# Kernel optimization log

Measured on AMD Instinct MI355X. Metric: run time of the kernel, lower is better.

Reference implementation:

```python
import jax, jax.numpy as jnp
import numpy as np

NEG_INF = -1e9  # masked_fill value from the torch module


def setup_inputs() -> dict:
    key = jax.random.key(0)
    ks = jax.random.split(key, 6)
    n_edges, hidden = 100000, 256
    n_paths, max_len = 20000, 16
    edge_emb = jax.random.normal(ks[0], (n_edges, hidden), dtype=jnp.float32)
    paths = jax.random.randint(ks[1], (n_paths, max_len), 0, n_edges)
    path_lens = jax.random.randint(ks[2], (n_paths,), 0, max_len)  # +1 in reference -> 1..max_len
    path_mask = jax.random.randint(ks[3], (n_paths,), 0, 2)
    # nn.Linear(hidden, 1) parameters
    W = jax.random.normal(ks[4], (1, hidden), dtype=jnp.float32) / np.sqrt(hidden)
    b = jax.random.normal(ks[5], (1,), dtype=jnp.float32) * 0.01
    return {"edge_emb": edge_emb, "paths": paths, "path_lens": path_lens,
            "path_mask": path_mask, "W": W, "b": b, "deterministic": 1}


def reference(edge_emb, paths, path_lens, path_mask, W, b, deterministic):
    # ragged per-path mean: emulate `for p in paths: edge_emb[p].mean(0)` with padded gather
    lens = path_lens + 1                                   # [P], 1..max_len
    pos = jnp.arange(paths.shape[1])                        # [L]
    valid = pos[None, :] < lens[:, None]                    # [P, L]
    gathered = edge_emb[paths]                              # [P, L, H]
    z = jnp.sum(jnp.where(valid[..., None], gathered, 0.0), axis=1) / lens[:, None].astype(edge_emb.dtype)  # [P, H]
    logits = z @ W[0] + b[0]                                # [P]  (Linear(H,1).squeeze())
    logits = jnp.where(path_mask == 0, NEG_INF, logits)
    logp = jax.nn.log_softmax(logits)
    if deterministic:
        p = jnp.argmax(logits)
    else:
        p = jax.random.categorical(jax.random.key(42), logits)
    logprob = logp[p]
    return (p, logprob, z[p])
```

## Files before the change

### kernel.cpp

```cpp
#include <hip/hip_runtime.h>
#include <math.h>

#define NEG_INF -1e9f

__global__ __launch_bounds__(256) void k_edge_dot(
    const float* __restrict__ emb, const float* __restrict__ W,
    float* __restrict__ s, int n_edges)
{
    int wave = (blockIdx.x * (int)blockDim.x + (int)threadIdx.x) >> 6;
    int lane = threadIdx.x & 63;
    if (wave >= n_edges) return;
    const float4 e = ((const float4*)emb)[wave * 64 + lane];
    const float4 w = ((const float4*)W)[lane];
    float d = e.x * w.x + e.y * w.y + e.z * w.z + e.w * w.w;
#pragma unroll
    for (int off = 32; off; off >>= 1) d += __shfl_down(d, off, 64);
    if (lane == 0) s[wave] = d;
}

__global__ __launch_bounds__(256) void k_logits16(
    const float* __restrict__ s, const int* __restrict__ paths,
    const int* __restrict__ path_lens, const int* __restrict__ path_mask,
    const float* __restrict__ b, float* __restrict__ logits, int n_paths)
{
    int p = blockIdx.x * (int)blockDim.x + (int)threadIdx.x;
    if (p >= n_paths) return;
    if (path_mask[p] == 0) { logits[p] = NEG_INF; return; }
    int len = path_lens[p] + 1;
    const int4* pp4 = (const int4*)(paths + (size_t)p * 16);
    int4 a0 = pp4[0], a1 = pp4[1], a2 = pp4[2], a3 = pp4[3];
    int idx[16] = { a0.x, a0.y, a0.z, a0.w, a1.x, a1.y, a1.z, a1.w,
                    a2.x, a2.y, a2.z, a2.w, a3.x, a3.y, a3.z, a3.w };
    float acc = 0.f;
#pragma unroll
    for (int j = 0; j < 16; ++j) {
        float v = s[idx[j]];
        acc += (j < len) ? v : 0.f;
    }
    logits[p] = acc / (float)len + b[0];
}

__global__ __launch_bounds__(256) void k_logits_gen(
    const float* __restrict__ s, const int* __restrict__ paths,
    const int* __restrict__ path_lens, const int* __restrict__ path_mask,
    const float* __restrict__ b, float* __restrict__ logits,
    int n_paths, int max_len)
{
    int p = blockIdx.x * (int)blockDim.x + (int)threadIdx.x;
    if (p >= n_paths) return;
    if (path_mask[p] == 0) { logits[p] = NEG_INF; return; }
    int len = path_lens[p] + 1;
    const int* pp = paths + (size_t)p * max_len;
    float acc = 0.f;
    for (int j = 0; j < len; ++j) acc += s[pp[j]];
    logits[p] = acc / (float)len + b[0];
}

__global__ __launch_bounds__(1024) void k_final(
    const float* __restrict__ logits, const float* __restrict__ emb,
    const int* __restrict__ paths, const int* __restrict__ path_lens,
    float* __restrict__ out, int n_paths, int max_len)
{
    __shared__ float sv[16];
    __shared__ int   si[16];
    __shared__ float ssum[16];
    __shared__ int   s_p, s_len;
    __shared__ float s_max, s_logprob;

    int tid = threadIdx.x, lane = tid & 63, wv = tid >> 6;
    int n4 = n_paths >> 2;
    const float4* l4 = (const float4*)logits;

    float bv = -INFINITY; int bi = 0x7fffffff;
    for (int i = tid; i < n4; i += 1024) {
        float4 v = l4[i];
        int base = i << 2;
        if (v.x > bv) { bv = v.x; bi = base; }
        if (v.y > bv) { bv = v.y; bi = base + 1; }
        if (v.z > bv) { bv = v.z; bi = base + 2; }
        if (v.w > bv) { bv = v.w; bi = base + 3; }
    }
    for (int i = (n4 << 2) + tid; i < n_paths; i += 1024) {
        float v = logits[i];
        if (v > bv) { bv = v; bi = i; }
    }
#pragma unroll
    for (int off = 32; off; off >>= 1) {
        float ov = __shfl_down(bv, off, 64);
        int   oi = __shfl_down(bi, off, 64);
        if (ov > bv || (ov == bv && oi < bi)) { bv = ov; bi = oi; }
    }
    if (lane == 0) { sv[wv] = bv; si[wv] = bi; }
    __syncthreads();
    if (tid == 0) {
        float mv = sv[0]; int mi = si[0];
        for (int w = 1; w < 16; ++w)
            if (sv[w] > mv || (sv[w] == mv && si[w] < mi)) { mv = sv[w]; mi = si[w]; }
        s_max = mv; s_p = mi; s_len = path_lens[mi] + 1;
    }
    __syncthreads();
    float mx = s_max;

    float se = 0.f;
    for (int i = tid; i < n4; i += 1024) {
        float4 v = l4[i];
        se += expf(v.x - mx) + expf(v.y - mx) + expf(v.z - mx) + expf(v.w - mx);
    }
    for (int i = (n4 << 2) + tid; i < n_paths; i += 1024)
        se += expf(logits[i] - mx);
#pragma unroll
    for (int off = 32; off; off >>= 1) se += __shfl_down(se, off, 64);
    if (lane == 0) ssum[wv] = se;
    __syncthreads();
    if (tid == 0) {
        float t = 0.f;
        for (int w = 0; w < 16; ++w) t += ssum[w];
        s_logprob = -logf(t);
    }
    __syncthreads();

    int p = s_p, len = s_len;
    if (tid < 256) {
        const int* pp = paths + (size_t)p * max_len;
        float acc = 0.f;
        for (int j = 0; j < len; ++j)
            acc += emb[(size_t)pp[j] * 256 + tid];
        out[2 + tid] = acc / (float)len;
    }
    if (tid == 0) { out[0] = (float)p; out[1] = s_logprob; }
}

extern "C" void kernel_launch(void* const* d_in, const int* in_sizes, int n_in,
                              void* d_out, int out_size, void* d_ws, size_t ws_size,
                              hipStream_t stream) {
    const float* emb       = (const float*)d_in[0];
    const int*   paths     = (const int*)  d_in[1];
    const int*   path_lens = (const int*)  d_in[2];
    const int*   path_mask = (const int*)  d_in[3];
    const float* W         = (const float*)d_in[4];
    const float* b         = (const float*)d_in[5];

    int hidden  = in_sizes[4];
    int n_edges = in_sizes[0] / hidden;
    int n_paths = in_sizes[2];
    int max_len = in_sizes[1] / n_paths;

    float* s      = (float*)d_ws;
    float* logits = s + n_edges;

    int blocks1 = (n_edges * 64 + 255) / 256;
    k_edge_dot<<<blocks1, 256, 0, stream>>>(emb, W, s, n_edges);

    int blocks2 = (n_paths + 255) / 256;
    if (max_len == 16)
        k_logits16<<<blocks2, 256, 0, stream>>>(s, paths, path_lens, path_mask,
                                                b, logits, n_paths);
    else
        k_logits_gen<<<blocks2, 256, 0, stream>>>(s, paths, path_lens, path_mask,
                                                  b, logits, n_paths, max_len);

    k_final<<<1, 1024, 0, stream>>>(logits, emb, paths, path_lens,
                                    (float*)d_out, n_paths, max_len);
}
```

Measured before the change: 167.3 us.

## Fuse logits and softmax/argmax reduction into one kernel with last-block finalize

Merges the per-path logits kernel and the single-block final reduction into one kernel. Each block computes a partial argmax, max and rescaled exp-sum and writes them to workspace, and an atomic counter picks the last block to combine the partials and gather the winning path's embedding mean. This removes a kernel launch, the logits round trip through memory and the serial single-block pass over all logits. In exchange it adds an atomic counter and threadfence, with the counter reset done inside the edge-dot kernel.

Result: no change. 166.0 us (-0.7%).

```diff
diff --git a/kernel.cpp b/kernel.cpp
--- a/kernel.cpp
+++ b/kernel.cpp
@@ -1,12 +1,14 @@
 #include <hip/hip_runtime.h>
 #include <math.h>
+#include <limits.h>
 
 #define NEG_INF -1e9f
 
 __global__ __launch_bounds__(256) void k_edge_dot(
     const float* __restrict__ emb, const float* __restrict__ W,
-    float* __restrict__ s, int n_edges)
+    float* __restrict__ s, int* __restrict__ counter, int n_edges)
 {
+    if (blockIdx.x == 0 && threadIdx.x == 0) *counter = 0;
     int wave = (blockIdx.x * (int)blockDim.x + (int)threadIdx.x) >> 6;
     int lane = threadIdx.x & 63;
     if (wave >= n_edges) return;
@@ -18,116 +20,125 @@
     if (lane == 0) s[wave] = d;
 }
 
-__global__ __launch_bounds__(256) void k_logits16(
+__global__ __launch_bounds__(256) void k_fused(
     const float* __restrict__ s, const int* __restrict__ paths,
     const int* __restrict__ path_lens, const int* __restrict__ path_mask,
-    const float* __restrict__ b, float* __restrict__ logits, int n_paths)
-{
-    int p = blockIdx.x * (int)blockDim.x + (int)threadIdx.x;
-    if (p >= n_paths) return;
-    if (path_mask[p] == 0) { logits[p] = NEG_INF; return; }
-    int len = path_lens[p] + 1;
-    const int4* pp4 = (const int4*)(paths + (size_t)p * 16);
-    int4 a0 = pp4[0], a1 = pp4[1], a2 = pp4[2], a3 = pp4[3];
-    int idx[16] = { a0.x, a0.y, a0.z, a0.w, a1.x, a1.y, a1.z, a1.w,
-                    a2.x, a2.y, a2.z, a2.w, a3.x, a3.y, a3.z, a3.w };
-    float acc = 0.f;
-#pragma unroll
-    for (int j = 0; j < 16; ++j) {
-        float v = s[idx[j]];
-        acc += (j < len) ? v : 0.f;
-    }
-    logits[p] = acc / (float)len + b[0];
-}
-
-__global__ __launch_bounds__(256) void k_logits_gen(
-    const float* __restrict__ s, const int* __restrict__ paths,
-    const int* __restrict__ path_lens, const int* __restrict__ path_mask,
-    const float* __restrict__ b, float* __restrict__ logits,
+    const float* __restrict__ b, const float* __restrict__ emb,
+    float* __restrict__ pmax, int* __restrict__ pidx, float* __restrict__ psum,
+    int* __restrict__ counter, float* __restrict__ out,
     int n_paths, int max_len)
 {
-    int p = blockIdx.x * (int)blockDim.x + (int)threadIdx.x;
-    if (p >= n_paths) return;
-    if (path_mask[p] == 0) { logits[p] = NEG_INF; return; }
-    int len = path_lens[p] + 1;
-    const int* pp = paths + (size_t)p * max_len;
-    float acc = 0.f;
-    for (int j = 0; j < len; ++j) acc += s[pp[j]];
-    logits[p] = acc / (float)len + b[0];
-}
+    __shared__ float rv[4];
+    __shared__ int   ri[4];
+    __shared__ float rs[4];
+    __shared__ float s_bm, s_M, s_S;
+    __shared__ int   s_bi, s_P, s_last;
 
-__global__ __launch_bounds__(1024) void k_final(
-    const float* __restrict__ logits, const float* __restrict__ emb,
-    const int* __restrict__ paths, const int* __restrict__ path_lens,
-    float* __restrict__ out, int n_paths, int max_len)
-{
-    __shared__ float sv[16];
-    __shared__ int   si[16];
-    __shared__ float ssum[16];
-    __shared__ int   s_p, s_len;
-    __shared__ float s_max, s_logprob;
+    const int tid = threadIdx.x, lane = tid & 63, wv = tid >> 6;
+    const int p = blockIdx.x * 256 + tid;
 
-    int tid = threadIdx.x, lane = tid & 63, wv = tid >> 6;
-    int n4 = n_paths >> 2;
-    const float4* l4 = (const float4*)logits;
+    float v = -INFINITY; int vi = INT_MAX;
+    if (p < n_paths) {
+        vi = p;
+        if (path_mask[p] == 0) {
+            v = NEG_INF;
+        } else {
+            int len = path_lens[p] + 1;
+            float acc = 0.f;
+            if (max_len == 16) {
+                const int4* pp4 = (const int4*)(paths + (size_t)p * 16);
+                int4 a0 = pp4[0], a1 = pp4[1], a2 = pp4[2], a3 = pp4[3];
+                int idx[16] = { a0.x, a0.y, a0.z, a0.w, a1.x, a1.y, a1.z, a1.w,
+                                a2.x, a2.y, a2.z, a2.w, a3.x, a3.y, a3.z, a3.w };
+#pragma unroll
+                for (int j = 0; j < 16; ++j) {
+                    float t = s[idx[j]];
+                    acc += (j < len) ? t : 0.f;
+                }
+            } else {
+                const int* pp = paths + (size_t)p * max_len;
+                for (int j = 0; j < len; ++j) acc += s[pp[j]];
+            }
+            v = acc / (float)len + b[0];
+        }
+    }
 
-    float bv = -INFINITY; int bi = 0x7fffffff;
-    for (int i = tid; i < n4; i += 1024) {
-        float4 v = l4[i];
-        int base = i << 2;
-        if (v.x > bv) { bv = v.x; bi = base; }
-        if (v.y > bv) { bv = v.y; bi = base + 1; }
-        if (v.z > bv) { bv = v.z; bi = base + 2; }
-        if (v.w > bv) { bv = v.w; bi = base + 3; }
-    }
-    for (int i = (n4 << 2) + tid; i < n_paths; i += 1024) {
-        float v = logits[i];
-        if (v > bv) { bv = v; bi = i; }
-    }
+    float bv = v; int bi = vi;
 #pragma unroll
     for (int off = 32; off; off >>= 1) {
         float ov = __shfl_down(bv, off, 64);
         int   oi = __shfl_down(bi, off, 64);
         if (ov > bv || (ov == bv && oi < bi)) { bv = ov; bi = oi; }
     }
-    if (lane == 0) { sv[wv] = bv; si[wv] = bi; }
+    if (lane == 0) { rv[wv] = bv; ri[wv] = bi; }
     __syncthreads();
     if (tid == 0) {
-        float mv = sv[0]; int mi = si[0];
-        for (int w = 1; w < 16; ++w)
-            if (sv[w] > mv || (sv[w] == mv && si[w] < mi)) { mv = sv[w]; mi = si[w]; }
-        s_max = mv; s_p = mi; s_len = path_lens[mi] + 1;
+        float mv = rv[0]; int mi = ri[0];
+        for (int w = 1; w < 4; ++w)
+            if (rv[w] > mv || (rv[w] == mv && ri[w] < mi)) { mv = rv[w]; mi = ri[w]; }
+        s_bm = mv; s_bi = mi;
     }
     __syncthreads();
-    float mx = s_max;
+    const float bm = s_bm;
 
-    float se = 0.f;
-    for (int i = tid; i < n4; i += 1024) {
-        float4 v = l4[i];
-        se += expf(v.x - mx) + expf(v.y - mx) + expf(v.z - mx) + expf(v.w - mx);
-    }
-    for (int i = (n4 << 2) + tid; i < n_paths; i += 1024)
-        se += expf(logits[i] - mx);
+    float se = expf(v - bm);
 #pragma unroll
     for (int off = 32; off; off >>= 1) se += __shfl_down(se, off, 64);
-    if (lane == 0) ssum[wv] = se;
+    if (lane == 0) rs[wv] = se;
+    __syncthreads();
+
+    if (tid == 0) {
+        pmax[blockIdx.x] = bm;
+        pidx[blockIdx.x] = s_bi;
+        psum[blockIdx.x] = rs[0] + rs[1] + rs[2] + rs[3];
+        __threadfence();
+        int tk = atomicAdd(counter, 1);
+        s_last = (tk == (int)gridDim.x - 1) ? 1 : 0;
+    }
+    __syncthreads();
+    if (!s_last) return;
+    __threadfence();
+
+    const int nb = gridDim.x;
+    float mv = -INFINITY; int mi = INT_MAX;
+    for (int i = tid; i < nb; i += 256) {
+        float t = pmax[i]; int ti = pidx[i];
+        if (t > mv || (t == mv && ti < mi)) { mv = t; mi = ti; }
+    }
+#pragma unroll
+    for (int off = 32; off; off >>= 1) {
+        float ov = __shfl_down(mv, off, 64);
+        int   oi = __shfl_down(mi, off, 64);
+        if (ov > mv || (ov == mv && oi < mi)) { mv = ov; mi = oi; }
+    }
+    if (lane == 0) { rv[wv] = mv; ri[wv] = mi; }
     __syncthreads();
     if (tid == 0) {
-        float t = 0.f;
-        for (int w = 0; w < 16; ++w) t += ssum[w];
-        s_logprob = -logf(t);
+        float M = rv[0]; int P = ri[0];
+        for (int w = 1; w < 4; ++w)
+            if (rv[w] > M || (rv[w] == M && ri[w] < P)) { M = rv[w]; P = ri[w]; }
+        s_M = M; s_P = P;
     }
     __syncthreads();
+    const float M = s_M; const int P = s_P;
 
-    int p = s_p, len = s_len;
-    if (tid < 256) {
-        const int* pp = paths + (size_t)p * max_len;
-        float acc = 0.f;
-        for (int j = 0; j < len; ++j)
-            acc += emb[(size_t)pp[j] * 256 + tid];
-        out[2 + tid] = acc / (float)len;
-    }
-    if (tid == 0) { out[0] = (float)p; out[1] = s_logprob; }
+    float sp = 0.f;
+    for (int i = tid; i < nb; i += 256)
+        sp += psum[i] * expf(pmax[i] - M);
+#pragma unroll
+    for (int off = 32; off; off >>= 1) sp += __shfl_down(sp, off, 64);
+    if (lane == 0) rs[wv] = sp;
+    __syncthreads();
+    if (tid == 0) s_S = rs[0] + rs[1] + rs[2] + rs[3];
+    __syncthreads();
+
+    const int lenP = path_lens[P] + 1;
+    const int* pp = paths + (size_t)P * max_len;
+    float acc = 0.f;
+    for (int j = 0; j < lenP; ++j)
+        acc += emb[(size_t)pp[j] * 256 + tid];
+    out[2 + tid] = acc / (float)lenP;
+    if (tid == 0) { out[0] = (float)P; out[1] = -logf(s_S); }
 }
 
 extern "C" void kernel_launch(void* const* d_in, const int* in_sizes, int n_in,
@@ -145,20 +156,18 @@
     int n_paths = in_sizes[2];
     int max_len = in_sizes[1] / n_paths;
 
-    float* s      = (float*)d_ws;
-    float* logits = s + n_edges;
+    int blocks2 = (n_paths + 255) / 256;
+
+    float* s       = (float*)d_ws;
+    float* pmax    = s + n_edges;
+    float* psum    = pmax + blocks2;
+    int*   pidx    = (int*)(psum + blocks2);
+    int*   counter = pidx + blocks2;
 
     int blocks1 = (n_edges * 64 + 255) / 256;
-    k_edge_dot<<<blocks1, 256, 0, stream>>>(emb, W, s, n_edges);
+    k_edge_dot<<<blocks1, 256, 0, stream>>>(emb, W, s, counter, n_edges);
 
-    int blocks2 = (n_paths + 255) / 256;
-    if (max_len == 16)
-        k_logits16<<<blocks2, 256, 0, stream>>>(s, paths, path_lens, path_mask,
-                                                b, logits, n_paths);
-    else
-        k_logits_gen<<<blocks2, 256, 0, stream>>>(s, paths, path_lens, path_mask,
-                                                  b, logits, n_paths, max_len);
-
-    k_final<<<1, 1024, 0, stream>>>(logits, emb, paths, path_lens,
-                                    (float*)d_out, n_paths, max_len);
+    k_fused<<<blocks2, 256, 0, stream>>>(s, paths, path_lens, path_mask, b, emb,
+                                         pmax, pidx, psum, counter,
+                                         (float*)d_out, n_paths, max_len);
 }
```
